# Optimization experiments

Hardware: AMD Instinct MI355X
Metric: run time of the kernel (lower is better)

The kernel has to match this reference:

```python
import jax, jax.numpy as jnp
import numpy as np

L, N, E = 2048, 2, 512
H = 8
HD = E // H
FF = 2048
NLAYERS = 2
EPS = 1e-5


def setup_inputs() -> dict:
    key = jax.random.key(0)
    ks = jax.random.split(key, 8)
    s = 0.02
    return {
        "src": jax.random.normal(ks[0], (L, N, E), jnp.float32),
        # packed qkv projection, torch Linear convention: y = x @ W.T + b
        "in_proj_w": jax.random.normal(ks[1], (NLAYERS, 3 * E, E), jnp.float32) * s,
        "in_proj_b": jnp.zeros((NLAYERS, 3 * E), jnp.float32),
        "out_proj_w": jax.random.normal(ks[2], (NLAYERS, E, E), jnp.float32) * s,
        "out_proj_b": jnp.zeros((NLAYERS, E), jnp.float32),
        "lin1_w": jax.random.normal(ks[3], (NLAYERS, FF, E), jnp.float32) * s,
        "lin1_b": jnp.zeros((NLAYERS, FF), jnp.float32),
        "lin2_w": jax.random.normal(ks[4], (NLAYERS, E, FF), jnp.float32) * s,
        "lin2_b": jnp.zeros((NLAYERS, E), jnp.float32),
        "ln1_g": jnp.ones((NLAYERS, E), jnp.float32),
        "ln1_b": jnp.zeros((NLAYERS, E), jnp.float32),
        "ln2_g": jnp.ones((NLAYERS, E), jnp.float32),
        "ln2_b": jnp.zeros((NLAYERS, E), jnp.float32),
    }


def _layer_norm(x, g, b):
    mu = jnp.mean(x, axis=-1, keepdims=True)
    var = jnp.mean(jnp.square(x - mu), axis=-1, keepdims=True)
    return (x - mu) * jax.lax.rsqrt(var + EPS) * g + b


def _mha(x, w_qkv, b_qkv, w_o, b_o):
    # x: [L, N, E] (seq-first, as in torch multi_head_attention_forward)
    qkv = jnp.einsum('lne,fe->lnf', x, w_qkv) + b_qkv  # [L, N, 3E]
    q, k, v = jnp.split(qkv, 3, axis=-1)
    q = q.reshape(L, N, H, HD) * (1.0 / np.sqrt(HD))  # torch scales q pre-bmm
    k = k.reshape(L, N, H, HD)
    v = v.reshape(L, N, H, HD)
    scores = jnp.einsum('lnhd,snhd->nhls', q, k)  # [N, H, L, S] -- O(L*S) matrix
    attn = jax.nn.softmax(scores, axis=-1)
    o = jnp.einsum('nhls,snhd->lnhd', attn, v).reshape(L, N, E)
    return jnp.einsum('lne,fe->lnf', o, w_o) + b_o


def reference(src, in_proj_w, in_proj_b, out_proj_w, out_proj_b,
              lin1_w, lin1_b, lin2_w, lin2_b, ln1_g, ln1_b, ln2_g, ln2_b):
    x = src
    for i in range(NLAYERS):  # fixed small layer count
        a = _mha(x, in_proj_w[i], in_proj_b[i], out_proj_w[i], out_proj_b[i])
        x = _layer_norm(x + a, ln1_g[i], ln1_b[i])  # post-norm (torch default)
        h = jax.nn.relu(jnp.einsum('lne,fe->lnf', x, lin1_w[i]) + lin1_b[i])
        f = jnp.einsum('lnf,ef->lne', h, lin2_w[i]) + lin2_b[i]
        x = _layer_norm(x + f, ln2_g[i], ln2_b[i])
    return x
```

## Files before the change

kernel.cpp:

```cpp
#include <hip/hip_runtime.h>
#include <hip/hip_bf16.h>

using bf16 = __hip_bfloat16;
typedef __bf16 bf16x8 __attribute__((ext_vector_type(8)));
typedef float f32x4 __attribute__((ext_vector_type(4)));

#define MFMA(a, b, c) __builtin_amdgcn_mfma_f32_16x16x32_bf16(a, b, c, 0, 0, 0)

constexpr int L = 2048, N = 2, E = 512, H = 8, HD = 64, FF = 2048;
constexpr int T = L * N;

__global__ void detect_dtype(const unsigned int* __restrict__ g,
                             int* __restrict__ flag) {
  if (threadIdx.x == 0 && blockIdx.x == 0)
    *flag = (g[0] != 0x3F800000u) ? 1 : 0;
}

__global__ __launch_bounds__(256) void cvt_to_bf16(
    const void* __restrict__ in, bf16* __restrict__ out, int n,
    const int* __restrict__ flag) {
  int i = (blockIdx.x * 256 + threadIdx.x) * 8;
  if (i >= n) return;
  if (*flag) {
    *(uint4*)&out[i] = *(const uint4*)&((const bf16*)in)[i];
  } else {
    float4 a = *(const float4*)&((const float*)in)[i];
    float4 b = *(const float4*)&((const float*)in)[i + 4];
    bf16 o8[8] = {__float2bfloat16(a.x), __float2bfloat16(a.y),
                  __float2bfloat16(a.z), __float2bfloat16(a.w),
                  __float2bfloat16(b.x), __float2bfloat16(b.y),
                  __float2bfloat16(b.z), __float2bfloat16(b.w)};
    *(uint4*)&out[i] = *(const uint4*)o8;
  }
}

__global__ __launch_bounds__(256) void cvt_to_f32(
    const void* __restrict__ in, float* __restrict__ out, int n,
    const int* __restrict__ flag) {
  int i = blockIdx.x * 256 + threadIdx.x;
  if (i >= n) return;
  out[i] = (*flag) ? __bfloat162float(((const bf16*)in)[i])
                   : ((const float*)in)[i];
}

__device__ __forceinline__ void gload16(const bf16* g, bf16* l) {
  __builtin_amdgcn_global_load_lds(
      (const __attribute__((address_space(1))) unsigned int*)g,
      (__attribute__((address_space(3))) unsigned int*)l, 16, 0, 0);
}

template <bool RELU, int BM, int BN>
__global__ __launch_bounds__(256) void gemm_bt(
    const bf16* __restrict__ A, const bf16* __restrict__ W,
    const float* __restrict__ bias, bf16* __restrict__ C,
    int M, int F, int K) {
  constexpr int SA = BM / 32;
  constexpr int SB = BN / 32;
  constexpr int MI = BM / 32;
  constexpr int NI = BN / 32;
  __shared__ __align__(16) bf16 As[2][BM * 64];
  __shared__ __align__(16) bf16 Bs[2][BN * 64];
  const int bm = blockIdx.x, bn = blockIdx.y;
  const int tid = threadIdx.x;
  const int w = tid >> 6, lane = tid & 63;
  const int wr = w >> 1, wc = w & 1;
  const int lhi = lane >> 4, llo = lane & 15;
  f32x4 acc[MI][NI] = {};

  const bf16 *ap[SA], *wp[SB];
#pragma unroll
  for (int s = 0; s < SA; ++s) {
    int c = tid + s * 256;
    int kg = c / BM, row = c % BM;
    ap[s] = &A[(size_t)(bm * BM + row) * K + kg * 8];
  }
#pragma unroll
  for (int s = 0; s < SB; ++s) {
    int c = tid + s * 256;
    int kg = c / BN, row = c % BN;
    wp[s] = &W[(size_t)(bn * BN + row) * K + kg * 8];
  }
  auto stage = [&](int buf, int k0) {
#pragma unroll
    for (int s = 0; s < SA; ++s)
      gload16(ap[s] + k0, &As[buf][(tid + s * 256) * 8]);
#pragma unroll
    for (int s = 0; s < SB; ++s)
      gload16(wp[s] + k0, &Bs[buf][(tid + s * 256) * 8]);
  };

  stage(0, 0);
  int cur = 0;
  for (int k0 = 0; k0 < K; k0 += 64) {
    __syncthreads();
    if (k0 + 64 < K) stage(cur ^ 1, k0 + 64);
    bf16x8 af[MI][2], bfr[NI][2];
#pragma unroll
    for (int mi = 0; mi < MI; ++mi)
#pragma unroll
      for (int ks = 0; ks < 2; ++ks)
        af[mi][ks] = *(const bf16x8*)&As[cur]
            [((ks * 4 + lhi) * BM + wr * (BM / 2) + mi * 16 + llo) * 8];
#pragma unroll
    for (int ni = 0; ni < NI; ++ni)
#pragma unroll
      for (int ks = 0; ks < 2; ++ks)
        bfr[ni][ks] = *(const bf16x8*)&Bs[cur]
            [((ks * 4 + lhi) * BN + wc * (BN / 2) + ni * 16 + llo) * 8];
    __builtin_amdgcn_s_setprio(1);
#pragma unroll
    for (int ks = 0; ks < 2; ++ks)
#pragma unroll
      for (int mi = 0; mi < MI; ++mi)
#pragma unroll
        for (int ni = 0; ni < NI; ++ni)
          acc[mi][ni] = MFMA(af[mi][ks], bfr[ni][ks], acc[mi][ni]);
    __builtin_amdgcn_s_setprio(0);
    cur ^= 1;
  }
#pragma unroll
  for (int mi = 0; mi < MI; ++mi) {
#pragma unroll
    for (int ni = 0; ni < NI; ++ni) {
      int col = bn * BN + wc * (BN / 2) + ni * 16 + llo;
      float bv = bias[col];
#pragma unroll
      for (int r = 0; r < 4; ++r) {
        int row = bm * BM + wr * (BM / 2) + mi * 16 + lhi * 4 + r;
        float v = acc[mi][ni][r] + bv;
        if (RELU) v = fmaxf(v, 0.f);
        C[(size_t)row * F + col] = __float2bfloat16(v);
      }
    }
  }
}

__global__ __launch_bounds__(256) void prep_kv(
    const bf16* __restrict__ qkv, bf16* __restrict__ kt,
    bf16* __restrict__ vt) {
  __shared__ __align__(16) bf16 Vl[64 * 72];
  const int blk = blockIdx.x;
  const int kb = blk & 31, nh = blk >> 5;
  const int n = nh >> 3, h = nh & 7;
  const int tid = threadIdx.x;
  bf16* ko = kt + ((size_t)nh * 32 + kb) * 4096;
  bf16* vo = vt + ((size_t)nh * 32 + kb) * 4096;
#pragma unroll
  for (int s = 0; s < 2; ++s) {
    int c = tid + s * 256;
    int jj = c >> 3, g = c & 7;
    size_t t = (size_t)((kb * 64 + jj) * N + n);
    uint4 kk = *(const uint4*)&qkv[t * 1536 + 512 + h * 64 + g * 8];
    *(uint4*)&ko[jj * 64 + ((g ^ (jj & 7)) * 8)] = kk;
    uint4 vv = *(const uint4*)&qkv[t * 1536 + 1024 + h * 64 + g * 8];
    *(uint4*)&Vl[jj * 72 + g * 8] = vv;
  }
  __syncthreads();
#pragma unroll
  for (int s = 0; s < 2; ++s) {
    int c = tid + s * 256;
    int d = c >> 3, gsw = c & 7;
    int g = gsw ^ (d & 7);
    bf16 tmp[8];
#pragma unroll
    for (int e = 0; e < 8; ++e) tmp[e] = Vl[(g * 8 + e) * 72 + d];
    *(uint4*)&vo[d * 64 + gsw * 8] = *(const uint4*)tmp;
  }
}

__global__ __launch_bounds__(256) void attn_split(
    const bf16* __restrict__ qkv, const bf16* __restrict__ kt,
    const bf16* __restrict__ vt, bf16* __restrict__ opart,
    float* __restrict__ lpart) {
  __shared__ __align__(16) bf16 Kb[2][4096];
  __shared__ __align__(16) bf16 Vb[2][4096];
  __shared__ __align__(16) bf16 Ps[64 * 72];
  const int blk = blockIdx.x;
  const int qb = blk & 31;
  const int nh = (blk >> 5) & 15;
  const int split = blk >> 9;
  const int n = nh >> 3, h = nh & 7;
  const int tid = threadIdx.x;
  const int w = tid >> 6, lane = tid & 63;
  const int lhi = lane >> 4, llo = lane & 15;
  const int kb0 = split * 8, kb1 = kb0 + 8;

#pragma unroll
  for (int s = 0; s < 2; ++s) {
    int c = tid + s * 256;
    int i = c >> 3, dc = c & 7;
    size_t t = (size_t)((qb * 64 + i) * N + n);
    *(uint4*)&Ps[i * 72 + dc * 8] =
        *(const uint4*)&qkv[t * 1536 + h * 64 + dc * 8];
  }
  __syncthreads();
  bf16x8 aq[2];
  aq[0] = *(const bf16x8*)&Ps[(w * 16 + llo) * 72 + 0 + lhi * 8];
  aq[1] = *(const bf16x8*)&Ps[(w * 16 + llo) * 72 + 32 + lhi * 8];

  const bf16* ktile = kt + (size_t)nh * 32 * 4096;
  const bf16* vtile = vt + (size_t)nh * 32 * 4096;
  auto stage = [&](int buf, int kb) {
#pragma unroll
    for (int s = 0; s < 2; ++s) {
      int c = tid + s * 256;
      gload16(ktile + (size_t)kb * 4096 + c * 8, &Kb[buf][c * 8]);
      gload16(vtile + (size_t)kb * 4096 + c * 8, &Vb[buf][c * 8]);
    }
  };
  stage(0, kb0);

  float psum[4] = {0.f, 0.f, 0.f, 0.f};
  f32x4 o[4] = {};
  int cur = 0;

  for (int kb = kb0; kb < kb1; ++kb) {
    __syncthreads();
    if (kb + 1 < kb1) stage(cur ^ 1, kb + 1);

    f32x4 sfr[4] = {};
    __builtin_amdgcn_s_setprio(1);
#pragma unroll
    for (int cb = 0; cb < 4; ++cb) {
      const int row = cb * 16 + llo;
#pragma unroll
      for (int ks = 0; ks < 2; ++ks) {
        bf16x8 b = *(const bf16x8*)&Kb[cur]
            [row * 64 + (((ks * 4 + lhi) ^ (row & 7)) << 3)];
        sfr[cb] = MFMA(aq[ks], b, sfr[cb]);
      }
    }
    __builtin_amdgcn_s_setprio(0);

#pragma unroll
    for (int cb = 0; cb < 4; ++cb) {
#pragma unroll
      for (int r = 0; r < 4; ++r) {
        float p = __expf(sfr[cb][r] * 0.125f);
        psum[r] += p;
        Ps[(w * 16 + lhi * 4 + r) * 72 + cb * 16 + llo] = __float2bfloat16(p);
      }
    }
    asm volatile("" ::: "memory");

    __builtin_amdgcn_s_setprio(1);
#pragma unroll
    for (int cb = 0; cb < 4; ++cb) {
      const int crow = cb * 16 + llo;
#pragma unroll
      for (int ks = 0; ks < 2; ++ks) {
        bf16x8 a =
            *(const bf16x8*)&Ps[(w * 16 + llo) * 72 + ks * 32 + lhi * 8];
        bf16x8 b = *(const bf16x8*)&Vb[cur]
            [crow * 64 + (((ks * 4 + lhi) ^ (crow & 7)) << 3)];
        o[cb] = MFMA(a, b, o[cb]);
      }
    }
    __builtin_amdgcn_s_setprio(0);
    cur ^= 1;
  }

#pragma unroll
  for (int r = 0; r < 4; ++r) {
    float v = psum[r];
#pragma unroll
    for (int d = 1; d < 16; d <<= 1) v += __shfl_xor(v, d);
    psum[r] = v;
  }
#pragma unroll
  for (int cb = 0; cb < 4; ++cb) {
#pragma unroll
    for (int r = 0; r < 4; ++r) {
      int i = w * 16 + lhi * 4 + r;
      int d = cb * 16 + llo;
      size_t t = (size_t)((qb * 64 + i) * N + n);
      opart[((size_t)split * T + t) * E + h * 64 + d] =
          __float2bfloat16(o[cb][r]);
    }
  }
  if (llo == 0) {
#pragma unroll
    for (int r = 0; r < 4; ++r) {
      int i = w * 16 + lhi * 4 + r;
      size_t t = (size_t)((qb * 64 + i) * N + n);
      lpart[(size_t)(split * T + t) * H + h] = psum[r];
    }
  }
}

__global__ __launch_bounds__(256) void attn_merge(
    const bf16* __restrict__ opart, const float* __restrict__ lpart,
    bf16* __restrict__ atn) {
  int i = (blockIdx.x * 256 + threadIdx.x) * 8;
  if (i >= T * E) return;
  int t = i >> 9, h = (i >> 6) & 7;
  float l = 0.f, acc[8] = {};
#pragma unroll
  for (int s = 0; s < 4; ++s) {
    l += lpart[(size_t)(s * T + t) * H + h];
    uint4 v = *(const uint4*)&opart[(size_t)s * T * E + i];
    const bf16* e8 = (const bf16*)&v;
#pragma unroll
    for (int e = 0; e < 8; ++e) acc[e] += __bfloat162float(e8[e]);
  }
  float rl = 1.f / l;
  bf16 r8[8];
#pragma unroll
  for (int e = 0; e < 8; ++e) r8[e] = __float2bfloat16(acc[e] * rl);
  *(uint4*)&atn[i] = *(const uint4*)r8;
}

template <typename OutT>
__global__ __launch_bounds__(256) void add_ln(
    const bf16* __restrict__ res, const bf16* __restrict__ y,
    const float* __restrict__ g, const float* __restrict__ b,
    OutT* __restrict__ out) {
  const int t = blockIdx.x;
  const int tid = threadIdx.x;
  const int w = tid >> 6, lane = tid & 63;
  const int e = tid * 2;
  const size_t base = (size_t)t * E;
  float v0 = __bfloat162float(res[base + e]) + __bfloat162float(y[base + e]);
  float v1 = __bfloat162float(res[base + e + 1]) + __bfloat162float(y[base + e + 1]);
  float s = v0 + v1, q = v0 * v0 + v1 * v1;
#pragma unroll
  for (int d = 1; d < 64; d <<= 1) {
    s += __shfl_xor(s, d);
    q += __shfl_xor(q, d);
  }
  __shared__ float rs[4], rq[4];
  if (lane == 0) { rs[w] = s; rq[w] = q; }
  __syncthreads();
  float S = rs[0] + rs[1] + rs[2] + rs[3];
  float Qq = rq[0] + rq[1] + rq[2] + rq[3];
  float mu = S * (1.f / E);
  float var = Qq * (1.f / E) - mu * mu;
  float rstd = rsqrtf(var + 1e-5f);
  float o0 = (v0 - mu) * rstd * g[e] + b[e];
  float o1 = (v1 - mu) * rstd * g[e + 1] + b[e + 1];
  if constexpr (__is_same(OutT, float)) {
    out[base + e] = o0;
    out[base + e + 1] = o1;
  } else {
    out[base + e] = __float2bfloat16(o0);
    out[base + e + 1] = __float2bfloat16(o1);
  }
}

extern "C" void kernel_launch(void* const* d_in, const int* in_sizes, int n_in,
                              void* d_out, int out_size, void* d_ws,
                              size_t ws_size, hipStream_t stream) {
  int* flag = (int*)d_ws;
  float* pbuf = (float*)((char*)d_ws + 16);
  float* in_b = pbuf;
  float* ob   = in_b + 3072;
  float* l1b  = ob + 1024;
  float* l2b  = l1b + 4096;
  float* ln1g = l2b + 1024;
  float* ln1b = ln1g + 1024;
  float* ln2g = ln1b + 1024;
  float* ln2b = ln2g + 1024;
  bf16* big  = (bf16*)(ln2b + 1024);
  bf16* srcb = big;
  bf16* in_w = srcb + (size_t)T * E;
  bf16* ow   = in_w + (size_t)2 * 1536 * E;
  bf16* l1w  = ow + (size_t)2 * E * E;
  bf16* l2w  = l1w + (size_t)2 * FF * E;
  bf16* qkv  = l2w + (size_t)2 * E * FF;
  bf16* atn  = qkv + (size_t)T * 1536;
  bf16* ybuf = atn + (size_t)T * E;
  bf16* x1   = ybuf + (size_t)T * E;
  bf16* x2   = x1 + (size_t)T * E;
  bf16* hbuf = x2 + (size_t)T * E;
  bf16* ktg  = hbuf + (size_t)T * FF;
  bf16* vtg  = ktg + (size_t)T * E;
  bf16* opart  = hbuf;
  float* lpart = (float*)ybuf;

  detect_dtype<<<1, 64, 0, stream>>>((const unsigned int*)d_in[9], flag);
  auto cvtb = [&](const void* in, bf16* out, int n) {
    cvt_to_bf16<<<dim3(n / 2048), 256, 0, stream>>>(in, out, n, flag);
  };
  auto cvtf = [&](const void* in, float* out, int n) {
    cvt_to_f32<<<dim3(n / 256), 256, 0, stream>>>(in, out, n, flag);
  };
  cvtb(d_in[0], srcb, T * E);
  cvtb(d_in[1], in_w, 2 * 1536 * E);
  cvtb(d_in[3], ow, 2 * E * E);
  cvtb(d_in[5], l1w, 2 * FF * E);
  cvtb(d_in[7], l2w, 2 * E * FF);
  cvtf(d_in[2], in_b, 3072);
  cvtf(d_in[4], ob, 1024);
  cvtf(d_in[6], l1b, 4096);
  cvtf(d_in[8], l2b, 1024);
  cvtf(d_in[9], ln1g, 1024);
  cvtf(d_in[10], ln1b, 1024);
  cvtf(d_in[11], ln2g, 1024);
  cvtf(d_in[12], ln2b, 1024);

  const bf16* x = srcb;
  for (int i = 0; i < 2; ++i) {
    gemm_bt<false, 128, 128><<<dim3(T / 128, 1536 / 128), 256, 0, stream>>>(
        x, in_w + (size_t)i * 1536 * E, in_b + i * 1536, qkv, T, 1536, E);
    prep_kv<<<dim3(512), 256, 0, stream>>>(qkv, ktg, vtg);
    attn_split<<<dim3(2048), 256, 0, stream>>>(qkv, ktg, vtg, opart, lpart);
    attn_merge<<<dim3(T * E / 2048), 256, 0, stream>>>(opart, lpart, atn);
    gemm_bt<false, 64, 64><<<dim3(T / 64, E / 64), 256, 0, stream>>>(
        atn, ow + (size_t)i * E * E, ob + i * E, ybuf, T, E, E);
    add_ln<bf16><<<dim3(T), 256, 0, stream>>>(
        x, ybuf, ln1g + i * E, ln1b + i * E, x1);
    gemm_bt<true, 128, 128><<<dim3(T / 128, FF / 128), 256, 0, stream>>>(
        x1, l1w + (size_t)i * FF * E, l1b + i * FF, hbuf, T, FF, E);
    gemm_bt<false, 64, 64><<<dim3(T / 64, E / 64), 256, 0, stream>>>(
        hbuf, l2w + (size_t)i * E * FF, l2b + i * E, ybuf, T, E, FF);
    if (i == 1) {
      add_ln<float><<<dim3(T), 256, 0, stream>>>(
          x1, ybuf, ln2g + i * E, ln2b + i * E, (float*)d_out);
    } else {
      add_ln<bf16><<<dim3(T), 256, 0, stream>>>(
          x1, ybuf, ln2g + i * E, ln2b + i * E, x2);
    }
    x = x2;
  }
}
```

Baseline: 330.4 us.

## Batch conversion launches, fuse residual into GEMM epilogue, retile GEMMs, remap attention blocks

```diff
diff --git a/kernel.cpp b/kernel.cpp
--- a/kernel.cpp
+++ b/kernel.cpp
@@ -16,31 +16,45 @@
     *flag = (g[0] != 0x3F800000u) ? 1 : 0;
 }
 
-__global__ __launch_bounds__(256) void cvt_to_bf16(
-    const void* __restrict__ in, bf16* __restrict__ out, int n,
-    const int* __restrict__ flag) {
-  int i = (blockIdx.x * 256 + threadIdx.x) * 8;
-  if (i >= n) return;
+struct CvtBigArgs {
+  const void* src[5];
+  bf16* dst[5];
+  int n[5];
+};
+__global__ __launch_bounds__(256) void cvt_big(CvtBigArgs a,
+                                               const int* __restrict__ flag) {
+  long long idx = (long long)(blockIdx.x * 256 + threadIdx.x) * 8;
+  int s = 0;
+  while (s < 5 && idx >= a.n[s]) { idx -= a.n[s]; ++s; }
+  if (s >= 5) return;
+  bf16* dst = a.dst[s];
   if (*flag) {
-    *(uint4*)&out[i] = *(const uint4*)&((const bf16*)in)[i];
+    *(uint4*)&dst[idx] = *(const uint4*)&((const bf16*)a.src[s])[idx];
   } else {
-    float4 a = *(const float4*)&((const float*)in)[i];
-    float4 b = *(const float4*)&((const float*)in)[i + 4];
-    bf16 o8[8] = {__float2bfloat16(a.x), __float2bfloat16(a.y),
-                  __float2bfloat16(a.z), __float2bfloat16(a.w),
-                  __float2bfloat16(b.x), __float2bfloat16(b.y),
-                  __float2bfloat16(b.z), __float2bfloat16(b.w)};
-    *(uint4*)&out[i] = *(const uint4*)o8;
-  }
-}
-
-__global__ __launch_bounds__(256) void cvt_to_f32(
-    const void* __restrict__ in, float* __restrict__ out, int n,
-    const int* __restrict__ flag) {
-  int i = blockIdx.x * 256 + threadIdx.x;
-  if (i >= n) return;
-  out[i] = (*flag) ? __bfloat162float(((const bf16*)in)[i])
-                   : ((const float*)in)[i];
+    const float* src = (const float*)a.src[s];
+    float4 x = *(const float4*)&src[idx];
+    float4 y = *(const float4*)&src[idx + 4];
+    bf16 o8[8] = {__float2bfloat16(x.x), __float2bfloat16(x.y),
+                  __float2bfloat16(x.z), __float2bfloat16(x.w),
+                  __float2bfloat16(y.x), __float2bfloat16(y.y),
+                  __float2bfloat16(y.z), __float2bfloat16(y.w)};
+    *(uint4*)&dst[idx] = *(const uint4*)o8;
+  }
+}
+
+struct CvtParArgs {
+  const void* src[8];
+  float* dst[8];
+  int n[8];
+};
+__global__ __launch_bounds__(256) void cvt_par(CvtParArgs a,
+                                               const int* __restrict__ flag) {
+  int idx = blockIdx.x * 256 + threadIdx.x;
+  int s = 0;
+  while (s < 8 && idx >= a.n[s]) { idx -= a.n[s]; ++s; }
+  if (s >= 8) return;
+  a.dst[s][idx] = (*flag) ? __bfloat162float(((const bf16*)a.src[s])[idx])
+                          : ((const float*)a.src[s])[idx];
 }
 
 __device__ __forceinline__ void gload16(const bf16* g, bf16* l) {
@@ -52,8 +66,8 @@
 template <bool RELU, int BM, int BN>
 __global__ __launch_bounds__(256) void gemm_bt(
     const bf16* __restrict__ A, const bf16* __restrict__ W,
-    const float* __restrict__ bias, bf16* __restrict__ C,
-    int M, int F, int K) {
+    const float* __restrict__ bias, const bf16* __restrict__ res,
+    bf16* __restrict__ C, int M, int F, int K) {
   constexpr int SA = BM / 32;
   constexpr int SB = BN / 32;
   constexpr int MI = BM / 32;
@@ -71,14 +85,12 @@
 #pragma unroll
   for (int s = 0; s < SA; ++s) {
     int c = tid + s * 256;
-    int kg = c / BM, row = c % BM;
-    ap[s] = &A[(size_t)(bm * BM + row) * K + kg * 8];
+    ap[s] = &A[(size_t)(bm * BM + c % BM) * K + (c / BM) * 8];
   }
 #pragma unroll
   for (int s = 0; s < SB; ++s) {
     int c = tid + s * 256;
-    int kg = c / BN, row = c % BN;
-    wp[s] = &W[(size_t)(bn * BN + row) * K + kg * 8];
+    wp[s] = &W[(size_t)(bn * BN + c % BN) * K + (c / BN) * 8];
   }
   auto stage = [&](int buf, int k0) {
 #pragma unroll
@@ -129,6 +141,7 @@
         int row = bm * BM + wr * (BM / 2) + mi * 16 + lhi * 4 + r;
         float v = acc[mi][ni][r] + bv;
         if (RELU) v = fmaxf(v, 0.f);
+        if (res) v += __bfloat162float(res[(size_t)row * F + col]);
         C[(size_t)row * F + col] = __float2bfloat16(v);
       }
     }
@@ -176,9 +189,10 @@
   __shared__ __align__(16) bf16 Vb[2][4096];
   __shared__ __align__(16) bf16 Ps[64 * 72];
   const int blk = blockIdx.x;
-  const int qb = blk & 31;
-  const int nh = (blk >> 5) & 15;
-  const int split = blk >> 9;
+  const int rest = blk >> 3;
+  const int nh = (blk & 7) * 2 + (rest & 1);
+  const int split = (rest >> 1) & 3;
+  const int qb = rest >> 3;
   const int n = nh >> 3, h = nh & 7;
   const int tid = threadIdx.x;
   const int w = tid >> 6, lane = tid & 63;
@@ -311,17 +325,16 @@
 }
 
 template <typename OutT>
-__global__ __launch_bounds__(256) void add_ln(
-    const bf16* __restrict__ res, const bf16* __restrict__ y,
-    const float* __restrict__ g, const float* __restrict__ b,
-    OutT* __restrict__ out) {
+__global__ __launch_bounds__(256) void ln_one(
+    const bf16* __restrict__ y, const float* __restrict__ g,
+    const float* __restrict__ b, OutT* __restrict__ out) {
   const int t = blockIdx.x;
   const int tid = threadIdx.x;
   const int w = tid >> 6, lane = tid & 63;
   const int e = tid * 2;
   const size_t base = (size_t)t * E;
-  float v0 = __bfloat162float(res[base + e]) + __bfloat162float(y[base + e]);
-  float v1 = __bfloat162float(res[base + e + 1]) + __bfloat162float(y[base + e + 1]);
+  float v0 = __bfloat162float(y[base + e]);
+  float v1 = __bfloat162float(y[base + e + 1]);
   float s = v0 + v1, q = v0 * v0 + v1 * v1;
 #pragma unroll
   for (int d = 1; d < 64; d <<= 1) {
@@ -378,47 +391,49 @@
   float* lpart = (float*)ybuf;
 
   detect_dtype<<<1, 64, 0, stream>>>((const unsigned int*)d_in[9], flag);
-  auto cvtb = [&](const void* in, bf16* out, int n) {
-    cvt_to_bf16<<<dim3(n / 2048), 256, 0, stream>>>(in, out, n, flag);
-  };
-  auto cvtf = [&](const void* in, float* out, int n) {
-    cvt_to_f32<<<dim3(n / 256), 256, 0, stream>>>(in, out, n, flag);
-  };
-  cvtb(d_in[0], srcb, T * E);
-  cvtb(d_in[1], in_w, 2 * 1536 * E);
-  cvtb(d_in[3], ow, 2 * E * E);
-  cvtb(d_in[5], l1w, 2 * FF * E);
-  cvtb(d_in[7], l2w, 2 * E * FF);
-  cvtf(d_in[2], in_b, 3072);
-  cvtf(d_in[4], ob, 1024);
-  cvtf(d_in[6], l1b, 4096);
-  cvtf(d_in[8], l2b, 1024);
-  cvtf(d_in[9], ln1g, 1024);
-  cvtf(d_in[10], ln1b, 1024);
-  cvtf(d_in[11], ln2g, 1024);
-  cvtf(d_in[12], ln2b, 1024);
+  CvtBigArgs ba;
+  ba.src[0] = d_in[0]; ba.dst[0] = srcb; ba.n[0] = T * E;
+  ba.src[1] = d_in[1]; ba.dst[1] = in_w; ba.n[1] = 2 * 1536 * E;
+  ba.src[2] = d_in[3]; ba.dst[2] = ow;   ba.n[2] = 2 * E * E;
+  ba.src[3] = d_in[5]; ba.dst[3] = l1w;  ba.n[3] = 2 * FF * E;
+  ba.src[4] = d_in[7]; ba.dst[4] = l2w;  ba.n[4] = 2 * E * FF;
+  int btot = ba.n[0] + ba.n[1] + ba.n[2] + ba.n[3] + ba.n[4];
+  cvt_big<<<dim3(btot / 2048), 256, 0, stream>>>(ba, flag);
+  CvtParArgs pa;
+  pa.src[0] = d_in[2];  pa.dst[0] = in_b; pa.n[0] = 3072;
+  pa.src[1] = d_in[4];  pa.dst[1] = ob;   pa.n[1] = 1024;
+  pa.src[2] = d_in[6];  pa.dst[2] = l1b;  pa.n[2] = 4096;
+  pa.src[3] = d_in[8];  pa.dst[3] = l2b;  pa.n[3] = 1024;
+  pa.src[4] = d_in[9];  pa.dst[4] = ln1g; pa.n[4] = 1024;
+  pa.src[5] = d_in[10]; pa.dst[5] = ln1b; pa.n[5] = 1024;
+  pa.src[6] = d_in[11]; pa.dst[6] = ln2g; pa.n[6] = 1024;
+  pa.src[7] = d_in[12]; pa.dst[7] = ln2b; pa.n[7] = 1024;
+  int ptot = 3072 + 1024 + 4096 + 1024 + 1024 * 4;
+  cvt_par<<<dim3(ptot / 256), 256, 0, stream>>>(pa, flag);
 
   const bf16* x = srcb;
   for (int i = 0; i < 2; ++i) {
-    gemm_bt<false, 128, 128><<<dim3(T / 128, 1536 / 128), 256, 0, stream>>>(
-        x, in_w + (size_t)i * 1536 * E, in_b + i * 1536, qkv, T, 1536, E);
+    gemm_bt<false, 64, 128><<<dim3(T / 64, 1536 / 128), 256, 0, stream>>>(
+        x, in_w + (size_t)i * 1536 * E, in_b + i * 1536, nullptr, qkv,
+        T, 1536, E);
     prep_kv<<<dim3(512), 256, 0, stream>>>(qkv, ktg, vtg);
     attn_split<<<dim3(2048), 256, 0, stream>>>(qkv, ktg, vtg, opart, lpart);
     attn_merge<<<dim3(T * E / 2048), 256, 0, stream>>>(opart, lpart, atn);
     gemm_bt<false, 64, 64><<<dim3(T / 64, E / 64), 256, 0, stream>>>(
-        atn, ow + (size_t)i * E * E, ob + i * E, ybuf, T, E, E);
-    add_ln<bf16><<<dim3(T), 256, 0, stream>>>(
-        x, ybuf, ln1g + i * E, ln1b + i * E, x1);
-    gemm_bt<true, 128, 128><<<dim3(T / 128, FF / 128), 256, 0, stream>>>(
-        x1, l1w + (size_t)i * FF * E, l1b + i * FF, hbuf, T, FF, E);
+        atn, ow + (size_t)i * E * E, ob + i * E, x, ybuf, T, E, E);
+    ln_one<bf16><<<dim3(T), 256, 0, stream>>>(
+        ybuf, ln1g + i * E, ln1b + i * E, x1);
+    gemm_bt<true, 64, 128><<<dim3(T / 64, FF / 128), 256, 0, stream>>>(
+        x1, l1w + (size_t)i * FF * E, l1b + i * FF, nullptr, hbuf,
+        T, FF, E);
     gemm_bt<false, 64, 64><<<dim3(T / 64, E / 64), 256, 0, stream>>>(
-        hbuf, l2w + (size_t)i * E * FF, l2b + i * E, ybuf, T, E, FF);
+        hbuf, l2w + (size_t)i * E * FF, l2b + i * E, x1, ybuf, T, E, FF);
     if (i == 1) {
-      add_ln<float><<<dim3(T), 256, 0, stream>>>(
-          x1, ybuf, ln2g + i * E, ln2b + i * E, (float*)d_out);
+      ln_one<float><<<dim3(T), 256, 0, stream>>>(
+          ybuf, ln2g + i * E, ln2b + i * E, (float*)d_out);
     } else {
-      add_ln<bf16><<<dim3(T), 256, 0, stream>>>(
-          x1, ybuf, ln2g + i * E, ln2b + i * E, x2);
+      ln_one<bf16><<<dim3(T), 256, 0, stream>>>(
+          ybuf, ln2g + i * E, ln2b + i * E, x2);
     }
     x = x2;
   }
```

Result: slower. 354.6 us (+7.3%).
